# Kernel tuning notes

Measured on AMD Instinct MI355X. Metric: run time of the kernel, lower is better.

The kernel has to match this reference:

```python
import jax, jax.numpy as jnp
import numpy as np

WH, WW = 7, 7
N = WH * WW
HEADS = 12
HEAD_DIM = 16
EMBED = 384
INNER = HEADS * HEAD_DIM
NW = 64
B_ = 2048
SCALE = HEAD_DIM ** -0.5


def _relative_position_index():
    ch, cw = np.meshgrid(np.arange(WH), np.arange(WW), indexing='ij')
    coords = np.stack([ch.ravel(), cw.ravel()])              # [2, N]
    rel = coords[:, :, None] - coords[:, None, :]             # [2, N, N]
    rel = rel.transpose(1, 2, 0)
    rel[:, :, 0] += WH - 1
    rel[:, :, 1] += WW - 1
    rel[:, :, 0] *= 2 * WW - 1
    return jnp.asarray(rel.sum(-1), dtype=jnp.int32)          # [N, N]


def setup_inputs() -> dict:
    key = jax.random.key(0)
    ks = jax.random.split(key, 8)
    s_in = EMBED ** -0.5
    s_inner = INNER ** -0.5
    x = jax.random.normal(ks[0], (B_, N, EMBED), jnp.float32)
    # Swin shift mask: 0 or -100 per window pair
    mbits = jax.random.bernoulli(ks[1], 0.2, (NW, N, N))
    mask = jnp.where(mbits, jnp.float32(-100.0), jnp.float32(0.0))
    return {
        'x': x,
        'mask': mask,
        'Wq': jax.random.normal(ks[2], (EMBED, INNER), jnp.float32) * s_in,
        'bq': jnp.zeros((INNER,), jnp.float32),
        'Wk': jax.random.normal(ks[3], (EMBED, INNER), jnp.float32) * s_in,
        'bk': jnp.zeros((INNER,), jnp.float32),
        'Wv': jax.random.normal(ks[4], (EMBED, INNER), jnp.float32) * s_in,
        'bv': jnp.zeros((INNER,), jnp.float32),
        'Wp': jax.random.normal(ks[5], (INNER, EMBED), jnp.float32) * s_inner,
        'bp': jnp.zeros((EMBED,), jnp.float32),
        'bias_table': jax.random.normal(ks[6], ((2 * WH - 1) * (2 * WW - 1), HEADS), jnp.float32) * 0.02,
        'rel_idx': _relative_position_index(),
    }


def reference(x, mask, Wq, bq, Wk, bk, Wv, bv, Wp, bp, bias_table, rel_idx):
    B, n, _ = x.shape
    q = (x @ Wq + bq).reshape(B, n, HEADS, HEAD_DIM)
    k = (x @ Wk + bk).reshape(B, n, HEADS, HEAD_DIM)
    v = (x @ Wv + bv).reshape(B, n, HEADS, HEAD_DIM)
    attn = jnp.einsum('bnhd,bmhd->bhnm', q * SCALE, k)        # [B, H, N, N]
    bias = bias_table[rel_idx]                                 # [N, N, H]
    attn = attn + jnp.transpose(bias, (2, 0, 1))[None]
    nW = mask.shape[0]
    attn = attn.reshape(B // nW, nW, HEADS, n, n) + mask[None, :, None]
    attn = jax.nn.softmax(attn.reshape(B, HEADS, n, n), axis=-1)
    out = jnp.einsum('bhnm,bmhd->bnhd', attn, v).reshape(B, n, INNER)
    return out @ Wp + bp
```

## Files before the change

kernel.cpp:

```cpp
#include <hip/hip_runtime.h>
#include <hip/hip_bf16.h>


typedef __attribute__((ext_vector_type(8))) short  bf8;
typedef __attribute__((ext_vector_type(4))) short  bf4;
typedef __attribute__((ext_vector_type(4))) float  f4;

#define L2E 1.4426950408889634f

union VU { unsigned u[2]; bf4 v; };

__device__ __forceinline__ short f2b(float f) {
  unsigned u = __builtin_bit_cast(unsigned, f);
  unsigned r = u + 0x7fffu + ((u >> 16) & 1u);
  return (short)(r >> 16);
}
__device__ __forceinline__ unsigned pk2(float lo, float hi) {
  unsigned short l = __builtin_bit_cast(unsigned short, __float2bfloat16(lo));
  unsigned short h = __builtin_bit_cast(unsigned short, __float2bfloat16(hi));
  return (unsigned)l | ((unsigned)h << 16);
}
__device__ __forceinline__ bf4 pkbf4(f4 v) {
  VU r; r.u[0] = pk2(v[0], v[1]); r.u[1] = pk2(v[2], v[3]);
  return r.v;
}
__device__ __forceinline__ float ex2(float x) {
#if __has_builtin(__builtin_amdgcn_exp2f)
  return __builtin_amdgcn_exp2f(x);
#else
  float r; asm("v_exp_f32 %0, %1" : "=v"(r) : "v"(x)); return r;
#endif
}
__device__ __forceinline__ f4 mfma16(bf4 a, bf4 b, f4 c) {
#if __has_builtin(__builtin_amdgcn_mfma_f32_16x16x16bf16_1k)
  return __builtin_amdgcn_mfma_f32_16x16x16bf16_1k(a, b, c, 0, 0, 0);
#else
  f4 d;
  asm("v_mfma_f32_16x16x16_bf16 %0, %1, %2, %3" : "=v"(d) : "v"(a), "v"(b), "v"(c));
  return d;
#endif
}

__global__ void wa_prep(const float* __restrict__ Wq, const float* __restrict__ Wk,
                        const float* __restrict__ Wv, const float* __restrict__ Wp,
                        const float* __restrict__ btab, const int* __restrict__ ridx,
                        const float* __restrict__ mask, int comb,
                        short* __restrict__ wt, short* __restrict__ wpt,
                        float* __restrict__ biasF, float* __restrict__ maskF,
                        float* __restrict__ combF) {
  int id = blockIdx.x * 256 + threadIdx.x;
  const int NWT = 576 * 384, NWP = 384 * 192;
  const int NBS = 12 * 64 * 64, NMS = 64 * 64 * 64, NCB = 64 * 12 * 64 * 64;
  if (id < NWT) {
    int row = id / 384, k = id - row * 384;
    int kind = row / 192, cc = row - kind * 192;
    const float* W = (kind == 0) ? Wq : (kind == 1 ? Wk : Wv);
    float v = W[k * 192 + cc];
    if (kind == 0) v *= 0.25f * L2E;
    wt[id] = f2b(v);
    return;
  }
  id -= NWT;
  if (id < NWP) {
    int n = id / 192, k = id - n * 192;
    wpt[id] = f2b(Wp[k * 384 + n]);
    return;
  }
  id -= NWP;
  if (comb) {
    if (id < NCB) {
      int win = id / 49152, rem = id - win * 49152;
      int h = rem >> 12, r2 = rem & 4095;
      int n = r2 >> 6, cc = r2 & 63;
      int m = (cc & 3) * 16 + (cc >> 2);
      float v;
      if (n >= 49)      v = -14427.0f;
      else if (m >= 49) v = 0.0f;
      else              v = (btab[ridx[m * 49 + n] * 12 + h]
                             + mask[win * 2401 + m * 49 + n]) * L2E;
      combF[id] = v;
    }
  } else {
    if (id < NBS) {
      int h = id >> 12, rem = id & 4095;
      int n = rem >> 6, cc = rem & 63;
      int m = (cc & 3) * 16 + (cc >> 2);
      float v;
      if (n >= 49)      v = -14427.0f;
      else if (m >= 49) v = 0.0f;
      else              v = btab[ridx[m * 49 + n] * 12 + h] * L2E;
      biasF[id] = v;
    } else if ((id -= NBS) < NMS) {
      int win = id >> 12, rem = id & 4095;
      int n = rem >> 6, cc = rem & 63;
      int m = (cc & 3) * 16 + (cc >> 2);
      maskF[id] = (m < 49 && n < 49) ? mask[win * 2401 + m * 49 + n] * L2E : 0.f;
    }
  }
}

struct __align__(16) Smem {
  union U {
    short xs[64][392];
    struct QK { short qs[64][200]; short ks[64][200]; } qk;
  } u;
};

template <bool COMB>
__global__ __launch_bounds__(256, 2)
void wa_main(const float* __restrict__ x,
             const float* __restrict__ bq, const float* __restrict__ bk,
             const float* __restrict__ bv, const float* __restrict__ bp,
             const short* __restrict__ wt, const short* __restrict__ wpt,
             const float* __restrict__ biasF, const float* __restrict__ maskF,
             const float* __restrict__ combF, float* __restrict__ out) {
  __shared__ Smem sm;
  const int tid = threadIdx.x;
  const int w   = tid >> 6;
  const int lid = tid & 63;
  const int g   = lid >> 4;
  const int c   = lid & 15;
  const int blk = blockIdx.x;
  const int mwin = (blk & 63) << 12;
  const int cwin = (blk & 63) * 49152;

  {
    const float* xw = x + (size_t)blk * 18816;
    f4 xv[18];
#pragma unroll
    for (int it = 0; it < 18; it++) {
      int i = tid + it * 256;
      xv[it] = *(const f4*)(xw + (i / 96) * 384 + (i % 96) * 4);
    }
    const int iT = tid + 18 * 256;
    f4 xt = {0.f, 0.f, 0.f, 0.f};
    if (iT < 4704) xt = *(const f4*)(xw + (iT / 96) * 384 + (iT % 96) * 4);
#pragma unroll
    for (int it = 0; it < 18; it++) {
      int i = tid + it * 256;
      *(bf4*)&sm.u.xs[i / 96][(i % 96) * 4] = pkbf4(xv[it]);
    }
    if (iT < 4704) *(bf4*)&sm.u.xs[iT / 96][(iT % 96) * 4] = pkbf4(xt);
    const bf8 zz = {0,0,0,0,0,0,0,0};
#pragma unroll
    for (int it = 0; it < 3; it++) {
      int i = tid + it * 256;
      if (i < 735) { int row = 49 + i / 49, c8 = (i % 49) * 8; *(bf8*)&sm.u.xs[row][c8] = zz; }
    }
  }
  __syncthreads();

  f4 acc[4][9];
#pragma unroll
  for (int mt = 0; mt < 4; mt++)
#pragma unroll
    for (int i = 0; i < 9; i++) acc[mt][i] = (f4){0.f, 0.f, 0.f, 0.f};
  int rowb[9];
#pragma unroll
  for (int i = 0; i < 9; i++) {
    int kind = i / 3, hh = 3 * w + i % 3;
    rowb[i] = (kind * 192 + hh * 16 + c) * 384;
  }
#pragma unroll 3
  for (int ks = 0; ks < 12; ks++) {
    const int k0 = ks * 32 + g * 8;
    bf8 a[4], b[9];
#pragma unroll
    for (int mt = 0; mt < 4; mt++) a[mt] = *(const bf8*)&sm.u.xs[mt * 16 + c][k0];
#pragma unroll
    for (int i = 0; i < 9; i++) b[i] = *(const bf8*)(wt + rowb[i] + k0);
#pragma unroll
    for (int mt = 0; mt < 4; mt++)
#pragma unroll
      for (int i = 0; i < 9; i++)
        acc[mt][i] = __builtin_amdgcn_mfma_f32_16x16x32_bf16(a[mt], b[i], acc[mt][i], 0, 0, 0);
  }
  __syncthreads();

  unsigned vpk[3][4][2];
#pragma unroll
  for (int i = 0; i < 9; i++) {
    const int kind = i / 3;
    const int col = (3 * w + i % 3) * 16 + c;
    const float bb = (kind == 0) ? (0.25f * L2E) * bq[col] : (kind == 1 ? bk[col] : bv[col]);
#pragma unroll
    for (int mt = 0; mt < 4; mt++) {
      unsigned w0 = pk2(acc[mt][i][0] + bb, acc[mt][i][1] + bb);
      unsigned w1 = pk2(acc[mt][i][2] + bb, acc[mt][i][3] + bb);
      if (kind == 2) {
        vpk[i - 6][mt][0] = w0;
        vpk[i - 6][mt][1] = w1;
      } else {
        short* dst = (kind == 0) ? &sm.u.qk.qs[0][0] : &sm.u.qk.ks[0][0];
        dst[(mt * 16 + g * 4 + 0) * 200 + col] = (short)(w0 & 0xFFFFu);
        dst[(mt * 16 + g * 4 + 1) * 200 + col] = (short)(w0 >> 16);
        dst[(mt * 16 + g * 4 + 2) * 200 + col] = (short)(w1 & 0xFFFFu);
        dst[(mt * 16 + g * 4 + 3) * 200 + col] = (short)(w1 >> 16);
      }
    }
  }

  const f4 z4 = {0.f, 0.f, 0.f, 0.f};
#pragma unroll
  for (int t = 0; t < 3; t++) {
    const int h  = 3 * w + t;
    const int hb = h * 16;
    bf4 afr[4], bfr[4];
#pragma unroll
    for (int nt = 0; nt < 4; nt++)
      afr[nt] = *(const bf4*)&sm.u.qk.ks[nt * 16 + c][hb + g * 4];
#pragma unroll
    for (int mt = 0; mt < 4; mt++)
      bfr[mt] = *(const bf4*)&sm.u.qk.qs[mt * 16 + c][hb + g * 4];
    f4 s[4][4];
#pragma unroll
    for (int nt = 0; nt < 4; nt++)
#pragma unroll
      for (int mt = 0; mt < 4; mt++)
        s[nt][mt] = mfma16(afr[nt], bfr[mt], z4);
    if (COMB) {
      const float* cbH = combF + cwin + (h << 12);
#pragma unroll
      for (int nt = 0; nt < 4; nt++)
#pragma unroll
        for (int r = 0; r < 4; r++) {
          const int n = nt * 16 + g * 4 + r;
          f4 cb4 = *(const f4*)&cbH[n * 64 + c * 4];
#pragma unroll
          for (int mt = 0; mt < 4; mt++)
            s[nt][mt][r] += cb4[mt];
        }
    } else {
      const float* bsH = biasF + (h << 12);
#pragma unroll
      for (int nt = 0; nt < 4; nt++)
#pragma unroll
        for (int r = 0; r < 4; r++) {
          const int n = nt * 16 + g * 4 + r;
          f4 b4 = *(const f4*)&bsH[n * 64 + c * 4];
          f4 m4 = *(const f4*)&maskF[mwin + n * 64 + c * 4];
#pragma unroll
          for (int mt = 0; mt < 4; mt++)
            s[nt][mt][r] += b4[mt] + m4[mt];
        }
    }
    float rin[4];
#pragma unroll
    for (int mt = 0; mt < 4; mt++) {
      float sum = 0.f;
#pragma unroll
      for (int nt = 0; nt < 4; nt++)
#pragma unroll
        for (int r = 0; r < 4; r++) {
          float p = ex2(s[nt][mt][r]);
          s[nt][mt][r] = p;
          sum += p;
        }
      sum += __shfl_xor(sum, 16, 64);
      sum += __shfl_xor(sum, 32, 64);
      rin[mt] = 1.f / sum;
    }
    unsigned ppk[4][4][2];
#pragma unroll
    for (int nt = 0; nt < 4; nt++)
#pragma unroll
      for (int mt = 0; mt < 4; mt++) {
        ppk[nt][mt][0] = pk2(s[nt][mt][0], s[nt][mt][1]);
        ppk[nt][mt][1] = pk2(s[nt][mt][2], s[nt][mt][3]);
      }
    f4 o[4];
#pragma unroll
    for (int mt = 0; mt < 4; mt++) o[mt] = z4;
#pragma unroll
    for (int kt = 0; kt < 4; kt++) {
      VU vu; vu.u[0] = vpk[t][kt][0]; vu.u[1] = vpk[t][kt][1];
#pragma unroll
      for (int mt = 0; mt < 4; mt++) {
        VU pu; pu.u[0] = ppk[kt][mt][0]; pu.u[1] = ppk[kt][mt][1];
        o[mt] = mfma16(vu.v, pu.v, o[mt]);
      }
    }
#pragma unroll
    for (int mt = 0; mt < 4; mt++) {
      f4 ov = o[mt] * rin[mt];
      *(bf4*)&sm.u.qk.qs[mt * 16 + c][hb + g * 4] = pkbf4(ov);
    }
  }

  bf8 wb0[6];
#pragma unroll
  for (int jt = 0; jt < 6; jt++)
    wb0[jt] = *(const bf8*)(wpt + (w * 96 + jt * 16 + c) * 192 + g * 8);
  __syncthreads();

  f4 acc3[6][4];
#pragma unroll
  for (int jt = 0; jt < 6; jt++)
#pragma unroll
    for (int mt = 0; mt < 4; mt++) acc3[jt][mt] = z4;
  {
    const int k0 = g * 8;
    bf8 ao[4];
#pragma unroll
    for (int mt = 0; mt < 4; mt++) ao[mt] = *(const bf8*)&sm.u.qk.qs[mt * 16 + c][k0];
#pragma unroll
    for (int jt = 0; jt < 6; jt++)
#pragma unroll
      for (int mt = 0; mt < 4; mt++)
        acc3[jt][mt] = __builtin_amdgcn_mfma_f32_16x16x32_bf16(wb0[jt], ao[mt], acc3[jt][mt], 0, 0, 0);
  }
#pragma unroll 2
  for (int ks3 = 1; ks3 < 6; ks3++) {
    const int k0 = ks3 * 32 + g * 8;
    bf8 ao[4], wb[6];
#pragma unroll
    for (int mt = 0; mt < 4; mt++) ao[mt] = *(const bf8*)&sm.u.qk.qs[mt * 16 + c][k0];
#pragma unroll
    for (int jt = 0; jt < 6; jt++)
      wb[jt] = *(const bf8*)(wpt + (w * 96 + jt * 16 + c) * 192 + k0);
#pragma unroll
    for (int jt = 0; jt < 6; jt++)
#pragma unroll
      for (int mt = 0; mt < 4; mt++)
        acc3[jt][mt] = __builtin_amdgcn_mfma_f32_16x16x32_bf16(wb[jt], ao[mt], acc3[jt][mt], 0, 0, 0);
  }
  float* ow = out + (size_t)blk * 18816;
#pragma unroll
  for (int jt = 0; jt < 6; jt++) {
    const int colb = w * 96 + jt * 16 + g * 4;
    const f4 bp4 = *(const f4*)&bp[colb];
#pragma unroll
    for (int mt = 0; mt < 4; mt++) {
      const int m = mt * 16 + c;
      if (m < 49) {
        f4 v = acc3[jt][mt] + bp4;
        *(f4*)&ow[m * 384 + colb] = v;
      }
    }
  }
}

extern "C" void kernel_launch(void* const* d_in, const int* in_sizes, int n_in,
                              void* d_out, int out_size, void* d_ws, size_t ws_size,
                              hipStream_t stream) {
  const float* x    = (const float*)d_in[0];
  const float* mask = (const float*)d_in[1];
  const float* Wq   = (const float*)d_in[2];
  const float* bq   = (const float*)d_in[3];
  const float* Wk   = (const float*)d_in[4];
  const float* bk   = (const float*)d_in[5];
  const float* Wv   = (const float*)d_in[6];
  const float* bv   = (const float*)d_in[7];
  const float* Wp   = (const float*)d_in[8];
  const float* bp   = (const float*)d_in[9];
  const float* btab = (const float*)d_in[10];
  const int*   ridx = (const int*)d_in[11];
  float* out = (float*)d_out;

  char* ws = (char*)d_ws;
  short* wt    = (short*)ws;
  short* wpt   = (short*)(ws + 442368);
  float* biasF = (float*)(ws + 589824);
  float* maskF = (float*)(ws + 786432);
  float* combF = (float*)(ws + 589824);

  const size_t NEED_COMB = 589824u + 64u * 12u * 64u * 64u * 4u;
  const int comb = (ws_size >= NEED_COMB) ? 1 : 0;

  if (comb) {
    const int NPREP = 576 * 384 + 384 * 192 + 64 * 12 * 64 * 64;
    wa_prep<<<dim3((NPREP + 255) / 256), dim3(256), 0, stream>>>(
        Wq, Wk, Wv, Wp, btab, ridx, mask, 1, wt, wpt, biasF, maskF, combF);
    wa_main<true><<<dim3(2048), dim3(256), 0, stream>>>(
        x, bq, bk, bv, bp, wt, wpt, biasF, maskF, combF, out);
  } else {
    const int NPREP = 576 * 384 + 384 * 192 + 12 * 64 * 64 + 64 * 64 * 64;
    wa_prep<<<dim3((NPREP + 255) / 256), dim3(256), 0, stream>>>(
        Wq, Wk, Wv, Wp, btab, ridx, mask, 0, wt, wpt, biasF, maskF, combF);
    wa_main<false><<<dim3(2048), dim3(256), 0, stream>>>(
        x, bq, bk, bv, bp, wt, wpt, biasF, maskF, combF, out);
  }
}
```

Measured before the change: 216.4 us.

## Split fused window attention into separate QKV-projection and attention kernels

Splits the single fused kernel into two: one computes the QKV projection and writes bf16 Q, K and a transposed V to global workspace, and one loads them and runs softmax attention plus the output projection. The attention kernel targets higher occupancy (launch bounds 3) and splits the output projection into two halves to reduce register pressure. In exchange it adds a global round-trip of about 150 MB of bf16 intermediates and an extra launch. The new path is taken only when the workspace is large enough.

```diff
diff --git a/kernel.cpp b/kernel.cpp
--- a/kernel.cpp
+++ b/kernel.cpp
@@ -99,12 +99,242 @@
   }
 }
 
+struct __align__(16) SmemA { short xs[64][392]; };
+struct __align__(16) SmemB { short qs[64][200]; short ks[64][200]; };
 struct __align__(16) Smem {
   union U {
     short xs[64][392];
     struct QK { short qs[64][200]; short ks[64][200]; } qk;
   } u;
 };
+
+__global__ __launch_bounds__(256, 2)
+void wa_qkv(const float* __restrict__ x,
+            const float* __restrict__ bq, const float* __restrict__ bk,
+            const float* __restrict__ bv, const short* __restrict__ wt,
+            short* __restrict__ qtg, short* __restrict__ ktg,
+            short* __restrict__ vtg) {
+  __shared__ SmemA sm;
+  const int tid = threadIdx.x;
+  const int w   = tid >> 6;
+  const int lid = tid & 63;
+  const int g   = lid >> 4;
+  const int c   = lid & 15;
+  const int blk = blockIdx.x;
+  {
+    const float* xw = x + (size_t)blk * 18816;
+    f4 xv[18];
+#pragma unroll
+    for (int it = 0; it < 18; it++) {
+      int i = tid + it * 256;
+      xv[it] = *(const f4*)(xw + (i / 96) * 384 + (i % 96) * 4);
+    }
+    const int iT = tid + 18 * 256;
+    f4 xt = {0.f, 0.f, 0.f, 0.f};
+    if (iT < 4704) xt = *(const f4*)(xw + (iT / 96) * 384 + (iT % 96) * 4);
+#pragma unroll
+    for (int it = 0; it < 18; it++) {
+      int i = tid + it * 256;
+      *(bf4*)&sm.xs[i / 96][(i % 96) * 4] = pkbf4(xv[it]);
+    }
+    if (iT < 4704) *(bf4*)&sm.xs[iT / 96][(iT % 96) * 4] = pkbf4(xt);
+    const bf8 zz = {0,0,0,0,0,0,0,0};
+#pragma unroll
+    for (int it = 0; it < 3; it++) {
+      int i = tid + it * 256;
+      if (i < 735) { int row = 49 + i / 49, c8 = (i % 49) * 8; *(bf8*)&sm.xs[row][c8] = zz; }
+    }
+  }
+  __syncthreads();
+
+  f4 acc[4][9];
+#pragma unroll
+  for (int mt = 0; mt < 4; mt++)
+#pragma unroll
+    for (int i = 0; i < 9; i++) acc[mt][i] = (f4){0.f, 0.f, 0.f, 0.f};
+  int rowb[9];
+#pragma unroll
+  for (int i = 0; i < 9; i++) {
+    int kind = i / 3, hh = 3 * w + i % 3;
+    rowb[i] = (kind * 192 + hh * 16 + c) * 384;
+  }
+#pragma unroll 3
+  for (int ks = 0; ks < 12; ks++) {
+    const int k0 = ks * 32 + g * 8;
+    bf8 a[4], b[9];
+#pragma unroll
+    for (int mt = 0; mt < 4; mt++) a[mt] = *(const bf8*)&sm.xs[mt * 16 + c][k0];
+#pragma unroll
+    for (int i = 0; i < 9; i++) b[i] = *(const bf8*)(wt + rowb[i] + k0);
+#pragma unroll
+    for (int mt = 0; mt < 4; mt++)
+#pragma unroll
+      for (int i = 0; i < 9; i++)
+        acc[mt][i] = __builtin_amdgcn_mfma_f32_16x16x32_bf16(a[mt], b[i], acc[mt][i], 0, 0, 0);
+  }
+
+  const size_t wb = (size_t)blk * 12288;
+#pragma unroll
+  for (int i = 0; i < 9; i++) {
+    const int kind = i / 3;
+    const int col = (3 * w + i % 3) * 16 + c;
+    const float bb = (kind == 0) ? (0.25f * L2E) * bq[col] : (kind == 1 ? bk[col] : bv[col]);
+#pragma unroll
+    for (int mt = 0; mt < 4; mt++) {
+      unsigned w0 = pk2(acc[mt][i][0] + bb, acc[mt][i][1] + bb);
+      unsigned w1 = pk2(acc[mt][i][2] + bb, acc[mt][i][3] + bb);
+      if (kind == 2) {
+        VU vv; vv.u[0] = w0; vv.u[1] = w1;
+        *(bf4*)&vtg[wb + (size_t)col * 64 + mt * 16 + g * 4] = vv.v;
+      } else {
+        short* dst = ((kind == 0) ? qtg : ktg) + wb;
+        dst[(mt * 16 + g * 4 + 0) * 192 + col] = (short)(w0 & 0xFFFFu);
+        dst[(mt * 16 + g * 4 + 1) * 192 + col] = (short)(w0 >> 16);
+        dst[(mt * 16 + g * 4 + 2) * 192 + col] = (short)(w1 & 0xFFFFu);
+        dst[(mt * 16 + g * 4 + 3) * 192 + col] = (short)(w1 >> 16);
+      }
+    }
+  }
+}
+
+__global__ __launch_bounds__(256, 3)
+void wa_attn(const short* __restrict__ qtg, const short* __restrict__ ktg,
+             const short* __restrict__ vtg, const short* __restrict__ wpt,
+             const float* __restrict__ combF, const float* __restrict__ bp,
+             float* __restrict__ out) {
+  __shared__ SmemB sm;
+  const int tid = threadIdx.x;
+  const int w   = tid >> 6;
+  const int lid = tid & 63;
+  const int g   = lid >> 4;
+  const int c   = lid & 15;
+  const int blk = blockIdx.x;
+  const size_t wb = (size_t)blk * 12288;
+  const int cwin = (blk & 63) * 49152;
+
+#pragma unroll
+  for (int it = 0; it < 6; it++) {
+    int i = tid + it * 256;
+    int row = i / 24, c8 = (i % 24) * 8;
+    *(bf8*)&sm.qs[row][c8] = *(const bf8*)&qtg[wb + row * 192 + c8];
+    *(bf8*)&sm.ks[row][c8] = *(const bf8*)&ktg[wb + row * 192 + c8];
+  }
+  __syncthreads();
+
+  const f4 z4 = {0.f, 0.f, 0.f, 0.f};
+#pragma unroll
+  for (int t = 0; t < 3; t++) {
+    const int h  = 3 * w + t;
+    const int hb = h * 16;
+    bf4 vf[4];
+#pragma unroll
+    for (int kt = 0; kt < 4; kt++)
+      vf[kt] = *(const bf4*)&vtg[wb + (size_t)(hb + c) * 64 + kt * 16 + g * 4];
+    bf4 afr[4], bfr[4];
+#pragma unroll
+    for (int nt = 0; nt < 4; nt++)
+      afr[nt] = *(const bf4*)&sm.ks[nt * 16 + c][hb + g * 4];
+#pragma unroll
+    for (int mt = 0; mt < 4; mt++)
+      bfr[mt] = *(const bf4*)&sm.qs[mt * 16 + c][hb + g * 4];
+    f4 s[4][4];
+#pragma unroll
+    for (int nt = 0; nt < 4; nt++)
+#pragma unroll
+      for (int mt = 0; mt < 4; mt++)
+        s[nt][mt] = mfma16(afr[nt], bfr[mt], z4);
+    const float* cbH = combF + cwin + (h << 12);
+#pragma unroll
+    for (int nt = 0; nt < 4; nt++)
+#pragma unroll
+      for (int r = 0; r < 4; r++) {
+        const int n = nt * 16 + g * 4 + r;
+        f4 cb4 = *(const f4*)&cbH[n * 64 + c * 4];
+#pragma unroll
+        for (int mt = 0; mt < 4; mt++)
+          s[nt][mt][r] += cb4[mt];
+      }
+    float rin[4];
+#pragma unroll
+    for (int mt = 0; mt < 4; mt++) {
+      float sum = 0.f;
+#pragma unroll
+      for (int nt = 0; nt < 4; nt++)
+#pragma unroll
+        for (int r = 0; r < 4; r++) {
+          float p = ex2(s[nt][mt][r]);
+          s[nt][mt][r] = p;
+          sum += p;
+        }
+      sum += __shfl_xor(sum, 16, 64);
+      sum += __shfl_xor(sum, 32, 64);
+      rin[mt] = 1.f / sum;
+    }
+    unsigned ppk[4][4][2];
+#pragma unroll
+    for (int nt = 0; nt < 4; nt++)
+#pragma unroll
+      for (int mt = 0; mt < 4; mt++) {
+        ppk[nt][mt][0] = pk2(s[nt][mt][0], s[nt][mt][1]);
+        ppk[nt][mt][1] = pk2(s[nt][mt][2], s[nt][mt][3]);
+      }
+    f4 o[4];
+#pragma unroll
+    for (int mt = 0; mt < 4; mt++) o[mt] = z4;
+#pragma unroll
+    for (int kt = 0; kt < 4; kt++) {
+#pragma unroll
+      for (int mt = 0; mt < 4; mt++) {
+        VU pu; pu.u[0] = ppk[kt][mt][0]; pu.u[1] = ppk[kt][mt][1];
+        o[mt] = mfma16(vf[kt], pu.v, o[mt]);
+      }
+    }
+#pragma unroll
+    for (int mt = 0; mt < 4; mt++) {
+      f4 ov = o[mt] * rin[mt];
+      *(bf4*)&sm.qs[mt * 16 + c][hb + g * 4] = pkbf4(ov);
+    }
+  }
+  __syncthreads();
+
+  float* ow = out + (size_t)blk * 18816;
+#pragma unroll 1
+  for (int half = 0; half < 2; half++) {
+    f4 acc3[3][4];
+#pragma unroll
+    for (int jt = 0; jt < 3; jt++)
+#pragma unroll
+      for (int mt = 0; mt < 4; mt++) acc3[jt][mt] = (f4){0.f, 0.f, 0.f, 0.f};
+#pragma unroll 2
+    for (int ks3 = 0; ks3 < 6; ks3++) {
+      const int k0 = ks3 * 32 + g * 8;
+      bf8 ao[4], wbr[3];
+#pragma unroll
+      for (int mt = 0; mt < 4; mt++) ao[mt] = *(const bf8*)&sm.qs[mt * 16 + c][k0];
+#pragma unroll
+      for (int jt = 0; jt < 3; jt++)
+        wbr[jt] = *(const bf8*)(wpt + (w * 96 + half * 48 + jt * 16 + c) * 192 + k0);
+#pragma unroll
+      for (int jt = 0; jt < 3; jt++)
+#pragma unroll
+        for (int mt = 0; mt < 4; mt++)
+          acc3[jt][mt] = __builtin_amdgcn_mfma_f32_16x16x32_bf16(wbr[jt], ao[mt], acc3[jt][mt], 0, 0, 0);
+    }
+#pragma unroll
+    for (int jt = 0; jt < 3; jt++) {
+      const int colb = w * 96 + half * 48 + jt * 16 + g * 4;
+      const f4 bp4 = *(const f4*)&bp[colb];
+#pragma unroll
+      for (int mt = 0; mt < 4; mt++) {
+        const int m = mt * 16 + c;
+        if (m < 49) {
+          f4 v = acc3[jt][mt] + bp4;
+          *(f4*)&ow[m * 384 + colb] = v;
+        }
+      }
+    }
+  }
+}
 
 template <bool COMB>
 __global__ __launch_bounds__(256, 2)
@@ -123,7 +353,6 @@
   const int blk = blockIdx.x;
   const int mwin = (blk & 63) << 12;
   const int cwin = (blk & 63) * 49152;
-
   {
     const float* xw = x + (size_t)blk * 18816;
     f4 xv[18];
@@ -149,7 +378,6 @@
     }
   }
   __syncthreads();
-
   f4 acc[4][9];
 #pragma unroll
   for (int mt = 0; mt < 4; mt++)
@@ -176,7 +404,6 @@
         acc[mt][i] = __builtin_amdgcn_mfma_f32_16x16x32_bf16(a[mt], b[i], acc[mt][i], 0, 0, 0);
   }
   __syncthreads();
-
   unsigned vpk[3][4][2];
 #pragma unroll
   for (int i = 0; i < 9; i++) {
@@ -199,7 +426,6 @@
       }
     }
   }
-
   const f4 z4 = {0.f, 0.f, 0.f, 0.f};
 #pragma unroll
   for (int t = 0; t < 3; t++) {
@@ -286,13 +512,11 @@
       *(bf4*)&sm.u.qk.qs[mt * 16 + c][hb + g * 4] = pkbf4(ov);
     }
   }
-
   bf8 wb0[6];
 #pragma unroll
   for (int jt = 0; jt < 6; jt++)
     wb0[jt] = *(const bf8*)(wpt + (w * 96 + jt * 16 + c) * 192 + g * 8);
   __syncthreads();
-
   f4 acc3[6][4];
 #pragma unroll
   for (int jt = 0; jt < 6; jt++)
@@ -312,17 +536,17 @@
 #pragma unroll 2
   for (int ks3 = 1; ks3 < 6; ks3++) {
     const int k0 = ks3 * 32 + g * 8;
-    bf8 ao[4], wb[6];
+    bf8 ao[4], wbr[6];
 #pragma unroll
     for (int mt = 0; mt < 4; mt++) ao[mt] = *(const bf8*)&sm.u.qk.qs[mt * 16 + c][k0];
 #pragma unroll
     for (int jt = 0; jt < 6; jt++)
-      wb[jt] = *(const bf8*)(wpt + (w * 96 + jt * 16 + c) * 192 + k0);
+      wbr[jt] = *(const bf8*)(wpt + (w * 96 + jt * 16 + c) * 192 + k0);
 #pragma unroll
     for (int jt = 0; jt < 6; jt++)
 #pragma unroll
       for (int mt = 0; mt < 4; mt++)
-        acc3[jt][mt] = __builtin_amdgcn_mfma_f32_16x16x32_bf16(wb[jt], ao[mt], acc3[jt][mt], 0, 0, 0);
+        acc3[jt][mt] = __builtin_amdgcn_mfma_f32_16x16x32_bf16(wbr[jt], ao[mt], acc3[jt][mt], 0, 0, 0);
   }
   float* ow = out + (size_t)blk * 18816;
 #pragma unroll
@@ -363,11 +587,20 @@
   float* biasF = (float*)(ws + 589824);
   float* maskF = (float*)(ws + 786432);
   float* combF = (float*)(ws + 589824);
-
-  const size_t NEED_COMB = 589824u + 64u * 12u * 64u * 64u * 4u;
-  const int comb = (ws_size >= NEED_COMB) ? 1 : 0;
-
-  if (comb) {
+  short* qtg   = (short*)(ws + 13172736);
+  short* ktg   = (short*)(ws + 63504384);
+  short* vtg   = (short*)(ws + 113836032);
+
+  const size_t NEED_COMB  = 13172736u;
+  const size_t NEED_SPLIT = 164167680u;
+
+  if (ws_size >= NEED_SPLIT) {
+    const int NPREP = 576 * 384 + 384 * 192 + 64 * 12 * 64 * 64;
+    wa_prep<<<dim3((NPREP + 255) / 256), dim3(256), 0, stream>>>(
+        Wq, Wk, Wv, Wp, btab, ridx, mask, 1, wt, wpt, biasF, maskF, combF);
+    wa_qkv<<<dim3(2048), dim3(256), 0, stream>>>(x, bq, bk, bv, wt, qtg, ktg, vtg);
+    wa_attn<<<dim3(2048), dim3(256), 0, stream>>>(qtg, ktg, vtg, wpt, combF, bp, out);
+  } else if (ws_size >= NEED_COMB) {
     const int NPREP = 576 * 384 + 384 * 192 + 64 * 12 * 64 * 64;
     wa_prep<<<dim3((NPREP + 255) / 256), dim3(256), 0, stream>>>(
         Wq, Wk, Wv, Wp, btab, ridx, mask, 1, wt, wpt, biasF, maskF, combF);
```

New measurement: 276.2 us. 27.6% more time.
